# Kernel optimization log

Measured on AMD Instinct MI355X. Metric: run time of the kernel, lower is better.

## Reference

```python
import jax, jax.numpy as jnp
import numpy as np
import math

B, S, E, H = 2, 2048, 1024, 16


def setup_inputs() -> dict:
    key = jax.random.key(0)
    ks = jax.random.split(key, 9)
    std = 0.02
    return {
        "x": jax.random.normal(ks[0], (B, S, E), dtype=jnp.float32),
        "Wq": jax.random.normal(ks[1], (E, E), dtype=jnp.float32) * std,
        "bq": jnp.zeros((E,), dtype=jnp.float32),
        "Wk": jax.random.normal(ks[2], (E, E), dtype=jnp.float32) * std,
        "bk": jnp.zeros((E,), dtype=jnp.float32),
        "Wv": jax.random.normal(ks[3], (E, E), dtype=jnp.float32) * std,
        "bv": jnp.zeros((E,), dtype=jnp.float32),
        "Wfc": jax.random.normal(ks[4], (E, E), dtype=jnp.float32) * std,
        "bfc": jnp.zeros((E,), dtype=jnp.float32),
        "n_head": H,
    }


def reference(x, Wq, bq, Wk, bk, Wv, bv, Wfc, bfc, n_head):
    Bn, Sn, En = x.shape
    Hd = En // n_head  # head_dim
    # torch Linear: y = x @ W.T + b
    def proj(W, b):
        return (x @ W.T + b).reshape(Bn, Sn, n_head, Hd).transpose(0, 2, 1, 3)  # [B,H,S,D]
    q = proj(Wq, bq)
    k = proj(Wk, bk)
    v = proj(Wv, bv)
    scores = jnp.einsum('bhqd,bhkd->bhqk', q, k) / math.sqrt(Hd)  # [B,H,S,S]
    # ALiBi: slopes_h = 2^{-(h+1)}; alibi[h,i,j] = -slope_h * (i - j)
    slopes = 2.0 ** (-jnp.arange(1, n_head + 1, dtype=jnp.float32))  # [H]
    pos = jnp.arange(Sn, dtype=jnp.float32)
    rel = pos[:, None] - pos[None, :]  # [S,S], memory_pos - context_pos
    alibi = -slopes[:, None, None] * rel  # [H,S,S]
    scores = scores + alibi[None]
    weights = jax.nn.softmax(scores, axis=-1)  # [B,H,S,S]
    out = jnp.einsum('bhqk,bhkd->bqhd', weights, v).reshape(Bn, Sn, En)
    out = out @ Wfc.T + bfc
    return (out, weights)
```

## Files before the change

kernel.cpp:

```cpp
#include <hip/hip_runtime.h>
#include <hip/hip_bf16.h>
#include <cstdint>
#include <cstddef>

#define BB 2
#define SS 2048
#define EE 1024
#define HH 16
#define MM (BB*SS)

typedef __bf16 bf16;
typedef __bf16 bf16x2 __attribute__((ext_vector_type(2)));
typedef __bf16 bf16x8 __attribute__((ext_vector_type(8)));
typedef float f32x4 __attribute__((ext_vector_type(4)));

#define GLD16(gsrc, ldst) \
  __builtin_amdgcn_global_load_lds((const __attribute__((address_space(1))) void*)(gsrc), \
                                   (__attribute__((address_space(3))) void*)(ldst), 16, 0, 0)

__global__ __launch_bounds__(256) void cvt_f32_bf16(const float* __restrict__ src,
                                                    bf16* __restrict__ dst, int n) {
    int i = (blockIdx.x * 256 + threadIdx.x) * 8;
    if (i >= n) return;
    float4 a = *(const float4*)(src + i);
    float4 b = *(const float4*)(src + i + 4);
    bf16 o[8] = {(bf16)a.x,(bf16)a.y,(bf16)a.z,(bf16)a.w,
                 (bf16)b.x,(bf16)b.y,(bf16)b.z,(bf16)b.w};
    *(uint4*)(dst + i) = *(uint4*)o;
}

__global__ __launch_bounds__(256) void cvt4(const float* __restrict__ a, const float* __restrict__ b,
                                            const float* __restrict__ c, const float* __restrict__ d,
                                            bf16* __restrict__ oa, bf16* __restrict__ ob,
                                            bf16* __restrict__ oc, bf16* __restrict__ od) {
    int sel = blockIdx.y;
    const float* s = sel == 0 ? a : sel == 1 ? b : sel == 2 ? c : d;
    bf16* o       = sel == 0 ? oa : sel == 1 ? ob : sel == 2 ? oc : od;
    int i = (blockIdx.x * 256 + threadIdx.x) * 8;
    float4 x = *(const float4*)(s + i);
    float4 y = *(const float4*)(s + i + 4);
    bf16 t[8] = {(bf16)x.x,(bf16)x.y,(bf16)x.z,(bf16)x.w,
                 (bf16)y.x,(bf16)y.y,(bf16)y.z,(bf16)y.w};
    *(uint4*)(o + i) = *(uint4*)t;
}

template<int MODE>
__global__ __launch_bounds__(256) void gemm128(const bf16* __restrict__ A,
                                               const bf16* __restrict__ W0,
                                               const bf16* __restrict__ W1,
                                               const bf16* __restrict__ W2,
                                               const float* __restrict__ b0,
                                               const float* __restrict__ b1,
                                               const float* __restrict__ b2,
                                               void* __restrict__ o0,
                                               void* __restrict__ o1,
                                               void* __restrict__ o2) {
    __shared__ bf16 Al[128*64];
    __shared__ bf16 Bl[128*64];
    const int t = threadIdx.x;
    const int wsel = blockIdx.x >> 3;
    const int n0 = (blockIdx.x & 7) * 128;
    const int m0 = blockIdx.y * 128;
    const bf16* W  = wsel == 0 ? W0 : wsel == 1 ? W1 : W2;
    const float* bias = wsel == 0 ? b0 : wsel == 1 ? b1 : b2;
    void* outp = wsel == 0 ? o0 : wsel == 1 ? o1 : o2;

    const int w = t >> 6, lane = t & 63, lg = lane >> 4, li = lane & 15;
    const int wr = w >> 1, wc = w & 1;
    f32x4 acc[4][4] = {};

    for (int k0 = 0; k0 < 1024; k0 += 64) {
        __syncthreads();
        #pragma unroll
        for (int i = 0; i < 4; ++i) {
            int f = i * 256 + t;
            int row = f >> 3, c = (f & 7) * 8;
            GLD16(A + (size_t)(m0 + row) * 1024 + k0 + c, Al + f * 8);
            GLD16(W + (size_t)(n0 + row) * 1024 + k0 + c, Bl + f * 8);
        }
        __syncthreads();
        #pragma unroll
        for (int ks = 0; ks < 2; ++ks) {
            bf16x8 af[4], bf_[4];
            #pragma unroll
            for (int m = 0; m < 4; ++m)
                af[m] = *(const bf16x8*)&Al[(wr*64 + m*16 + li)*64 + ks*32 + lg*8];
            #pragma unroll
            for (int n = 0; n < 4; ++n)
                bf_[n] = *(const bf16x8*)&Bl[(wc*64 + n*16 + li)*64 + ks*32 + lg*8];
            #pragma unroll
            for (int m = 0; m < 4; ++m)
                #pragma unroll
                for (int n = 0; n < 4; ++n)
                    acc[m][n] = __builtin_amdgcn_mfma_f32_16x16x32_bf16(af[m], bf_[n], acc[m][n], 0,0,0);
        }
    }
    #pragma unroll
    for (int m = 0; m < 4; ++m)
      #pragma unroll
      for (int n = 0; n < 4; ++n)
        #pragma unroll
        for (int r = 0; r < 4; ++r) {
            int row = m0 + wr*64 + m*16 + lg*4 + r;
            int col = n0 + wc*64 + n*16 + li;
            float v = acc[m][n][r] + bias[col];
            if (MODE == 0) {
                int b = row >> 11, s = row & (SS-1);
                int h = col >> 6, d = col & 63;
                ((bf16*)outp)[(((size_t)(b*HH + h)*SS + s) << 6) + d] = (bf16)v;
            } else {
                ((float*)outp)[(size_t)row*1024 + col] = v;
            }
        }
}

__global__ __launch_bounds__(256) void transpose_v(const bf16* __restrict__ V,
                                                   bf16* __restrict__ Vt) {
    __shared__ bf16 L[64][72];
    const int bh = blockIdx.y, s0 = blockIdx.x * 64, t = threadIdx.x;
    for (int id = t; id < 512; id += 256) {
        int row = id >> 3, c = id & 7;
        *(uint4*)&L[row][c*8] = *(const uint4*)&V[((size_t)bh*SS + s0 + row)*64 + c*8];
    }
    __syncthreads();
    for (int id = t; id < 512; id += 256) {
        int d = id >> 3, c = id & 7;
        bf16 tmp[8];
        #pragma unroll
        for (int jj = 0; jj < 8; ++jj) tmp[jj] = L[c*8 + jj][d];
        *(uint4*)&Vt[((size_t)bh*64 + d)*SS + s0 + c*8] = *(uint4*)tmp;
    }
}

__global__ __launch_bounds__(256) void attn_kernel(const bf16* __restrict__ Q,
                                                   const bf16* __restrict__ Kk,
                                                   const bf16* __restrict__ Vt,
                                                   float* __restrict__ wout,
                                                   bf16* __restrict__ aout) {
    __shared__ bf16 Ks[64*64];
    __shared__ bf16 Vs[64*64];
    __shared__ bf16 Ps[64*64];
    char* Ksb = (char*)Ks;
    char* Vsb = (char*)Vs;
    char* Psb = (char*)Ps;

    const int qt = blockIdx.x, bh = blockIdx.y;
    const int b = bh >> 4, h = bh & 15;
    const int q0 = qt * 64;
    const int t = threadIdx.x, w = t >> 6, lane = t & 63, lg = lane >> 4, li = lane & 15;
    const float slope = exp2f(-(float)(h + 1));
    const size_t kvbase = (size_t)bh * SS * 64;
    const size_t vtbase = (size_t)bh * 64 * SS;

    const bf16* qptr = Q + kvbase + (size_t)(q0 + w*16 + li) * 64;
    bf16x8 aq0 = *(const bf16x8*)(qptr + lg*8);
    bf16x8 aq1 = *(const bf16x8*)(qptr + 32 + lg*8);

    const float qf = (float)(q0 + w*16 + li);
    const int swz = (li & 7) << 4;
    float m = -1e30f, l = 0.f;

    for (int kt = 0; kt < 32; ++kt) {
        const int j0 = kt * 64;
        __syncthreads();
        #pragma unroll
        for (int i = 0; i < 2; ++i) {
            int f = i * 256 + t;
            int row = f >> 3, c16 = f & 7;
            GLD16(Kk + kvbase + (size_t)(j0 + row)*64 + (c16 ^ (row & 7))*8, Ks + f*8);
        }
        __syncthreads();
        f32x4 sc[4] = {};
        #pragma unroll
        for (int cb = 0; cb < 4; ++cb) {
            int row = cb*16 + li;
            bf16x8 bk0 = *(const bf16x8*)(Ksb + row*128 + ((     lg*16) ^ swz));
            bf16x8 bk1 = *(const bf16x8*)(Ksb + row*128 + ((64 + lg*16) ^ swz));
            sc[cb] = __builtin_amdgcn_mfma_f32_16x16x32_bf16(bk0, aq0, sc[cb], 0,0,0);
            sc[cb] = __builtin_amdgcn_mfma_f32_16x16x32_bf16(bk1, aq1, sc[cb], 0,0,0);
        }
        float s[4][4];
        float tmax = -1e30f;
        #pragma unroll
        for (int cb = 0; cb < 4; ++cb) {
            float jb = (float)(j0 + cb*16 + lg*4);
            #pragma unroll
            for (int r = 0; r < 4; ++r) {
                float v = sc[cb][r]*0.125f + slope*((jb + (float)r) - qf);
                s[cb][r] = v;
                tmax = fmaxf(tmax, v);
            }
        }
        tmax = fmaxf(tmax, __shfl_xor(tmax, 16));
        tmax = fmaxf(tmax, __shfl_xor(tmax, 32));
        float mnew = fmaxf(m, tmax);
        float rs = 0.f;
        #pragma unroll
        for (int cb = 0; cb < 4; ++cb)
            #pragma unroll
            for (int r = 0; r < 4; ++r)
                rs += __expf(s[cb][r] - mnew);
        rs += __shfl_xor(rs, 16);
        rs += __shfl_xor(rs, 32);
        l = l * __expf(m - mnew) + rs;
        m = mnew;
    }
    const float rinv = 1.f / l;

    f32x4 acc[4] = {};
    float* wrow = wout + ((size_t)bh*SS + q0 + w*16 + li) * SS;
    const int prow = w*16 + li;
    for (int kt = 0; kt < 32; ++kt) {
        const int j0 = kt * 64;
        __syncthreads();
        #pragma unroll
        for (int i = 0; i < 2; ++i) {
            int f = i * 256 + t;
            int row = f >> 3, c16 = f & 7;
            GLD16(Kk + kvbase + (size_t)(j0 + row)*64 + (c16 ^ (row & 7))*8, Ks + f*8);
            GLD16(Vt + vtbase + (size_t)row*SS + j0 + (c16 ^ (row & 7))*8,   Vs + f*8);
        }
        __syncthreads();
        f32x4 sc[4] = {};
        #pragma unroll
        for (int cb = 0; cb < 4; ++cb) {
            int row = cb*16 + li;
            bf16x8 bk0 = *(const bf16x8*)(Ksb + row*128 + ((     lg*16) ^ swz));
            bf16x8 bk1 = *(const bf16x8*)(Ksb + row*128 + ((64 + lg*16) ^ swz));
            sc[cb] = __builtin_amdgcn_mfma_f32_16x16x32_bf16(bk0, aq0, sc[cb], 0,0,0);
            sc[cb] = __builtin_amdgcn_mfma_f32_16x16x32_bf16(bk1, aq1, sc[cb], 0,0,0);
        }
        #pragma unroll
        for (int cb = 0; cb < 4; ++cb) {
            float jb = (float)(j0 + cb*16 + lg*4);
            float4 wv;
            wv.x = __expf(sc[cb][0]*0.125f + slope*((jb + 0.f) - qf) - m) * rinv;
            wv.y = __expf(sc[cb][1]*0.125f + slope*((jb + 1.f) - qf) - m) * rinv;
            wv.z = __expf(sc[cb][2]*0.125f + slope*((jb + 2.f) - qf) - m) * rinv;
            wv.w = __expf(sc[cb][3]*0.125f + slope*((jb + 3.f) - qf) - m) * rinv;
            *(float4*)&wrow[j0 + cb*16 + lg*4] = wv;
            bf16x2 p01 = {(bf16)wv.x, (bf16)wv.y};
            bf16x2 p23 = {(bf16)wv.z, (bf16)wv.w};
            uint2 u;
            u.x = __builtin_bit_cast(unsigned, p01);
            u.y = __builtin_bit_cast(unsigned, p23);
            *(uint2*)(Psb + prow*128 + ((cb*32 + lg*8) ^ swz)) = u;
        }
        #pragma unroll
        for (int ks = 0; ks < 2; ++ks) {
            bf16x8 ap = *(const bf16x8*)(Psb + prow*128 + ((ks*64 + lg*16) ^ swz));
            #pragma unroll
            for (int d0 = 0; d0 < 4; ++d0) {
                int vrow = d0*16 + li;
                bf16x8 bv = *(const bf16x8*)(Vsb + vrow*128 + ((ks*64 + lg*16) ^ swz));
                acc[d0] = __builtin_amdgcn_mfma_f32_16x16x32_bf16(ap, bv, acc[d0], 0,0,0);
            }
        }
    }
    #pragma unroll
    for (int d0 = 0; d0 < 4; ++d0)
        #pragma unroll
        for (int r = 0; r < 4; ++r) {
            int srow = q0 + w*16 + lg*4 + r;
            aout[((size_t)(b*SS + srow))*EE + h*64 + d0*16 + li] = (bf16)acc[d0][r];
        }
}

extern "C" void kernel_launch(void* const* d_in, const int* in_sizes, int n_in,
                              void* d_out, int out_size, void* d_ws, size_t ws_size,
                              hipStream_t stream) {
    const float* x   = (const float*)d_in[0];
    const float* Wq  = (const float*)d_in[1];
    const float* bq  = (const float*)d_in[2];
    const float* Wk  = (const float*)d_in[3];
    const float* bk  = (const float*)d_in[4];
    const float* Wv  = (const float*)d_in[5];
    const float* bv  = (const float*)d_in[6];
    const float* Wfc = (const float*)d_in[7];
    const float* bfc = (const float*)d_in[8];

    char* ws = (char*)d_ws;
    const size_t MB = 1024u*1024u;
    bf16* xb  = (bf16*)(ws + 0);
    bf16* wqb = (bf16*)(ws + 8*MB);
    bf16* wkb = (bf16*)(ws + 10*MB);
    bf16* wvb = (bf16*)(ws + 12*MB);
    bf16* wfb = (bf16*)(ws + 14*MB);
    bf16* Qb  = (bf16*)(ws + 16*MB);
    bf16* Kb  = (bf16*)(ws + 24*MB);
    bf16* Vb  = (bf16*)(ws + 32*MB);
    bf16* Vtb = (bf16*)(ws + 40*MB);
    bf16* Ab  = (bf16*)(ws + 48*MB);

    float* outp = (float*)d_out;
    float* wout = outp + (size_t)BB*SS*EE;

    cvt_f32_bf16<<<dim3(4194304/8/256), 256, 0, stream>>>(x, xb, 4194304);
    cvt4<<<dim3(512, 4), 256, 0, stream>>>(Wq, Wk, Wv, Wfc, wqb, wkb, wvb, wfb);

    gemm128<0><<<dim3(24, 32), 256, 0, stream>>>(xb, wqb, wkb, wvb, bq, bk, bv, Qb, Kb, Vb);

    transpose_v<<<dim3(SS/64, BB*HH), 256, 0, stream>>>(Vb, Vtb);

    attn_kernel<<<dim3(SS/64, BB*HH), 256, 0, stream>>>(Qb, Kb, Vtb, wout, Ab);

    gemm128<1><<<dim3(8, 32), 256, 0, stream>>>(Ab, wfb, wfb, wfb, bfc, bfc, bfc, d_out, d_out, d_out);
}
```

Measured before the change: 298.6 us.

## Drop online max via ALiBi bound, double-buffer K, read K/V directly in pass two

The first pass no longer tracks a running row max. It uses a fixed per-column offset derived from the ALiBi bias (j minus SS-1) with base-2 exponentials and incrementally updated bias terms, and the log of the sum is folded into the exponent for pass two. The first pass double-buffers K tiles in shared memory so one barrier per iteration remains. The second pass drops shared-memory staging and barriers for K and V and loads MFMA operands straight from global memory. The fixed offset relies on raw scores staying small enough to avoid overflow or underflow, and the uncached global reads may raise memory traffic.

```diff
diff --git a/kernel.cpp b/kernel.cpp
--- a/kernel.cpp
+++ b/kernel.cpp
@@ -137,11 +137,8 @@
                                                    const bf16* __restrict__ Vt,
                                                    float* __restrict__ wout,
                                                    bf16* __restrict__ aout) {
-    __shared__ bf16 Ks[64*64];
-    __shared__ bf16 Vs[64*64];
+    __shared__ bf16 Ks[2][64*64];
     __shared__ bf16 Ps[64*64];
-    char* Ksb = (char*)Ks;
-    char* Vsb = (char*)Vs;
     char* Psb = (char*)Ps;
 
     const int qt = blockIdx.x, bh = blockIdx.y;
@@ -151,25 +148,42 @@
     const float slope = exp2f(-(float)(h + 1));
     const size_t kvbase = (size_t)bh * SS * 64;
     const size_t vtbase = (size_t)bh * 64 * SS;
+    const float L2E = 1.4426950408889634f;
+    const float K1 = 0.125f * L2E;
+    const float C  = slope * L2E;
+    const float C64 = C * 64.f;
 
     const bf16* qptr = Q + kvbase + (size_t)(q0 + w*16 + li) * 64;
     bf16x8 aq0 = *(const bf16x8*)(qptr + lg*8);
     bf16x8 aq1 = *(const bf16x8*)(qptr + 32 + lg*8);
 
-    const float qf = (float)(q0 + w*16 + li);
     const int swz = (li & 7) << 4;
-    float m = -1e30f, l = 0.f;
-
+    float ecr[4][4];
+    #pragma unroll
+    for (int cb = 0; cb < 4; ++cb)
+        #pragma unroll
+        for (int r = 0; r < 4; ++r)
+            ecr[cb][r] = C * (float)(cb*16 + lg*4 + r - (SS-1));
+
+    float l = 0.f;
+
+    #pragma unroll
+    for (int i = 0; i < 2; ++i) {
+        int f = i*256 + t; int row = f >> 3, c16 = f & 7;
+        GLD16(Kk + kvbase + (size_t)row*64 + (c16 ^ (row & 7))*8, &Ks[0][0] + f*8);
+    }
+    __syncthreads();
     for (int kt = 0; kt < 32; ++kt) {
-        const int j0 = kt * 64;
-        __syncthreads();
-        #pragma unroll
-        for (int i = 0; i < 2; ++i) {
-            int f = i * 256 + t;
-            int row = f >> 3, c16 = f & 7;
-            GLD16(Kk + kvbase + (size_t)(j0 + row)*64 + (c16 ^ (row & 7))*8, Ks + f*8);
-        }
-        __syncthreads();
+        const int cur = kt & 1;
+        if (kt + 1 < 32) {
+            #pragma unroll
+            for (int i = 0; i < 2; ++i) {
+                int f = i*256 + t; int row = f >> 3, c16 = f & 7;
+                GLD16(Kk + kvbase + (size_t)((kt+1)*64 + row)*64 + (c16 ^ (row & 7))*8,
+                      &Ks[cur^1][0] + f*8);
+            }
+        }
+        const char* Ksb = (const char*)&Ks[cur][0];
         f32x4 sc[4] = {};
         #pragma unroll
         for (int cb = 0; cb < 4; ++cb) {
@@ -179,65 +193,48 @@
             sc[cb] = __builtin_amdgcn_mfma_f32_16x16x32_bf16(bk0, aq0, sc[cb], 0,0,0);
             sc[cb] = __builtin_amdgcn_mfma_f32_16x16x32_bf16(bk1, aq1, sc[cb], 0,0,0);
         }
-        float s[4][4];
-        float tmax = -1e30f;
-        #pragma unroll
-        for (int cb = 0; cb < 4; ++cb) {
-            float jb = (float)(j0 + cb*16 + lg*4);
+        #pragma unroll
+        for (int cb = 0; cb < 4; ++cb)
             #pragma unroll
             for (int r = 0; r < 4; ++r) {
-                float v = sc[cb][r]*0.125f + slope*((jb + (float)r) - qf);
-                s[cb][r] = v;
-                tmax = fmaxf(tmax, v);
+                l += __builtin_amdgcn_exp2f(fmaf(sc[cb][r], K1, ecr[cb][r]));
+                ecr[cb][r] += C64;
             }
-        }
-        tmax = fmaxf(tmax, __shfl_xor(tmax, 16));
-        tmax = fmaxf(tmax, __shfl_xor(tmax, 32));
-        float mnew = fmaxf(m, tmax);
-        float rs = 0.f;
-        #pragma unroll
-        for (int cb = 0; cb < 4; ++cb)
-            #pragma unroll
-            for (int r = 0; r < 4; ++r)
-                rs += __expf(s[cb][r] - mnew);
-        rs += __shfl_xor(rs, 16);
-        rs += __shfl_xor(rs, 32);
-        l = l * __expf(m - mnew) + rs;
-        m = mnew;
-    }
-    const float rinv = 1.f / l;
+        __syncthreads();
+    }
+    l += __shfl_xor(l, 16);
+    l += __shfl_xor(l, 32);
+    const float lgl = __builtin_amdgcn_logf(l);
+
+    #pragma unroll
+    for (int cb = 0; cb < 4; ++cb)
+        #pragma unroll
+        for (int r = 0; r < 4; ++r)
+            ecr[cb][r] = C * (float)(cb*16 + lg*4 + r - (SS-1)) - lgl;
 
     f32x4 acc[4] = {};
     float* wrow = wout + ((size_t)bh*SS + q0 + w*16 + li) * SS;
     const int prow = w*16 + li;
     for (int kt = 0; kt < 32; ++kt) {
         const int j0 = kt * 64;
-        __syncthreads();
-        #pragma unroll
-        for (int i = 0; i < 2; ++i) {
-            int f = i * 256 + t;
-            int row = f >> 3, c16 = f & 7;
-            GLD16(Kk + kvbase + (size_t)(j0 + row)*64 + (c16 ^ (row & 7))*8, Ks + f*8);
-            GLD16(Vt + vtbase + (size_t)row*SS + j0 + (c16 ^ (row & 7))*8,   Vs + f*8);
-        }
-        __syncthreads();
+        const bf16* kb_ = Kk + kvbase + (size_t)j0 * 64;
+        const bf16* vb_ = Vt + vtbase + j0;
         f32x4 sc[4] = {};
         #pragma unroll
         for (int cb = 0; cb < 4; ++cb) {
-            int row = cb*16 + li;
-            bf16x8 bk0 = *(const bf16x8*)(Ksb + row*128 + ((     lg*16) ^ swz));
-            bf16x8 bk1 = *(const bf16x8*)(Ksb + row*128 + ((64 + lg*16) ^ swz));
-            sc[cb] = __builtin_amdgcn_mfma_f32_16x16x32_bf16(bk0, aq0, sc[cb], 0,0,0);
-            sc[cb] = __builtin_amdgcn_mfma_f32_16x16x32_bf16(bk1, aq1, sc[cb], 0,0,0);
+            const bf16* kr = kb_ + (size_t)(cb*16 + li)*64;
+            bf16x8 ak0 = *(const bf16x8*)(kr + lg*8);
+            bf16x8 ak1 = *(const bf16x8*)(kr + 32 + lg*8);
+            sc[cb] = __builtin_amdgcn_mfma_f32_16x16x32_bf16(ak0, aq0, sc[cb], 0,0,0);
+            sc[cb] = __builtin_amdgcn_mfma_f32_16x16x32_bf16(ak1, aq1, sc[cb], 0,0,0);
         }
         #pragma unroll
         for (int cb = 0; cb < 4; ++cb) {
-            float jb = (float)(j0 + cb*16 + lg*4);
             float4 wv;
-            wv.x = __expf(sc[cb][0]*0.125f + slope*((jb + 0.f) - qf) - m) * rinv;
-            wv.y = __expf(sc[cb][1]*0.125f + slope*((jb + 1.f) - qf) - m) * rinv;
-            wv.z = __expf(sc[cb][2]*0.125f + slope*((jb + 2.f) - qf) - m) * rinv;
-            wv.w = __expf(sc[cb][3]*0.125f + slope*((jb + 3.f) - qf) - m) * rinv;
+            wv.x = __builtin_amdgcn_exp2f(fmaf(sc[cb][0], K1, ecr[cb][0]));
+            wv.y = __builtin_amdgcn_exp2f(fmaf(sc[cb][1], K1, ecr[cb][1]));
+            wv.z = __builtin_amdgcn_exp2f(fmaf(sc[cb][2], K1, ecr[cb][2]));
+            wv.w = __builtin_amdgcn_exp2f(fmaf(sc[cb][3], K1, ecr[cb][3]));
             *(float4*)&wrow[j0 + cb*16 + lg*4] = wv;
             bf16x2 p01 = {(bf16)wv.x, (bf16)wv.y};
             bf16x2 p23 = {(bf16)wv.z, (bf16)wv.w};
@@ -245,14 +242,15 @@
             u.x = __builtin_bit_cast(unsigned, p01);
             u.y = __builtin_bit_cast(unsigned, p23);
             *(uint2*)(Psb + prow*128 + ((cb*32 + lg*8) ^ swz)) = u;
+            ecr[cb][0] += C64; ecr[cb][1] += C64;
+            ecr[cb][2] += C64; ecr[cb][3] += C64;
         }
         #pragma unroll
         for (int ks = 0; ks < 2; ++ks) {
             bf16x8 ap = *(const bf16x8*)(Psb + prow*128 + ((ks*64 + lg*16) ^ swz));
             #pragma unroll
             for (int d0 = 0; d0 < 4; ++d0) {
-                int vrow = d0*16 + li;
-                bf16x8 bv = *(const bf16x8*)(Vsb + vrow*128 + ((ks*64 + lg*16) ^ swz));
+                bf16x8 bv = *(const bf16x8*)(vb_ + (size_t)(d0*16 + li)*SS + ks*32 + lg*8);
                 acc[d0] = __builtin_amdgcn_mfma_f32_16x16x32_bf16(ap, bv, acc[d0], 0,0,0);
             }
         }
```

Result: slower. 415.9 us (+39.3%).
